# Optimization experiments

Measured on AMD Instinct MI355X. Metric: run time of the kernel, lower is better.

Reference implementation:

```python
import jax, jax.numpy as jnp
import numpy as np

B, T, U, D, H, V = 2, 512, 128, 512, 512, 1024

def setup_inputs() -> dict:
    key = jax.random.key(0)
    k1, k2, k3, k4 = jax.random.split(key, 4)
    pred_inp = jax.random.normal(k1, (B, U, D), dtype=jnp.float32)
    enc_inp = jax.random.normal(k2, (B, T, D), dtype=jnp.float32)
    W0 = jax.random.normal(k3, (D, H), dtype=jnp.float32) * (1.0 / np.sqrt(D))
    b0 = jnp.zeros((H,), dtype=jnp.float32)
    W1 = jax.random.normal(k4, (H, V), dtype=jnp.float32) * (1.0 / np.sqrt(H))
    b1 = jnp.zeros((V,), dtype=jnp.float32)
    return {"pred_inp": pred_inp, "enc_inp": enc_inp, "W0": W0, "b0": b0, "W1": W1, "b1": b1}

def reference(pred_inp, enc_inp, W0, b0, W1, b1):
    # broadcast-add: enc [B,T,1,D] + pred [B,1,U,D] -> [B,T,U,D]
    x = enc_inp[:, :, None, :] + pred_inp[:, None, :, :]
    # Dense(additional_size)
    h = jnp.einsum('btud,dh->btuh', x, W0) + b0
    # Dense(output_size)
    out = jnp.einsum('btuh,hv->btuv', h, W1) + b1
    return out
```

## Files before the change

### kernel.cpp

```cpp
#include <hip/hip_runtime.h>


typedef float vf4 __attribute__((ext_vector_type(4)));
typedef short bf16x8 __attribute__((ext_vector_type(8)));
typedef float f32x4 __attribute__((ext_vector_type(4)));
typedef unsigned short us4 __attribute__((ext_vector_type(4)));

#define PADK 40

__device__ __forceinline__ unsigned short f2bf(float f) {
    union { float f; unsigned u; } v; v.f = f;
    const unsigned r = v.u + 0x7FFFu + ((v.u >> 16) & 1u);
    return (unsigned short)(r >> 16);
}

template<bool A_BF16, bool C_BF16>
__global__ __launch_bounds__(256) void gemm_mfma(
    const void* __restrict__ Aptr, const float* __restrict__ A1,
    const float* __restrict__ Bmat,
    const float* __restrict__ biasv,
    void* __restrict__ Cptr, int N, int K)
{
    __shared__ unsigned short As[64 * PADK];
    __shared__ unsigned short Bst[64 * PADK];

    const int tid  = threadIdx.x;
    const int row0 = blockIdx.y * 64;
    const int col0 = blockIdx.x * 64;
    const int w    = tid >> 6;
    const int lane = tid & 63;
    const int l16  = lane & 15;
    const int kq   = lane >> 4;

    float4 ar[2]; bf16x8 ab; float4 br[2];

    auto loadA = [&](int kb) {
        if (A_BF16) {
            const unsigned short* A = (const unsigned short*)Aptr;
            const int r = tid >> 2, k8 = (tid & 3) << 3;
            ab = *reinterpret_cast<const bf16x8*>(A + (size_t)(row0 + r) * K + kb + k8);
        } else {
            #pragma unroll
            for (int i = 0; i < 2; ++i) {
                const int idx = tid + (i << 8);
                const int r = idx >> 3, k4 = (idx & 7) << 2;
                const float* Arow = (row0 < 1024)
                    ? (const float*)Aptr + (size_t)(row0 + r) * K
                    : A1 + (size_t)(row0 - 1024 + r) * K;
                ar[i] = *reinterpret_cast<const float4*>(Arow + kb + k4);
            }
        }
    };
    auto loadB = [&](int kb) {
        #pragma unroll
        for (int i = 0; i < 2; ++i) {
            const int idx = tid + (i << 8);
            const int kk = idx >> 4, n4 = (idx & 15) << 2;
            br[i] = *reinterpret_cast<const float4*>(Bmat + (size_t)(kb + kk) * N + col0 + n4);
        }
    };
    auto stage = [&]() {
        if (A_BF16) {
            const int r = tid >> 2, k8 = (tid & 3) << 3;
            *reinterpret_cast<bf16x8*>(&As[r * PADK + k8]) = ab;
        } else {
            #pragma unroll
            for (int i = 0; i < 2; ++i) {
                const int idx = tid + (i << 8);
                const int r = idx >> 3, k4 = (idx & 7) << 2;
                us4 p = { f2bf(ar[i].x), f2bf(ar[i].y), f2bf(ar[i].z), f2bf(ar[i].w) };
                *reinterpret_cast<us4*>(&As[r * PADK + k4]) = p;
            }
        }
        #pragma unroll
        for (int i = 0; i < 2; ++i) {
            const int idx = tid + (i << 8);
            const int kk = idx >> 4, n4 = (idx & 15) << 2;
            Bst[(n4 + 0) * PADK + kk] = f2bf(br[i].x);
            Bst[(n4 + 1) * PADK + kk] = f2bf(br[i].y);
            Bst[(n4 + 2) * PADK + kk] = f2bf(br[i].z);
            Bst[(n4 + 3) * PADK + kk] = f2bf(br[i].w);
        }
    };

    f32x4 acc[4] = {};
    const unsigned short* a_base = &As[(w * 16 + l16) * PADK + kq * 8];

    loadA(0); loadB(0);
    const int nkt = K >> 5;
    for (int kt = 0; kt < nkt; ++kt) {
        __syncthreads();
        stage();
        __syncthreads();
        if (kt + 1 < nkt) { loadA((kt + 1) << 5); loadB((kt + 1) << 5); }
        bf16x8 a = *reinterpret_cast<const bf16x8*>(a_base);
        #pragma unroll
        for (int nf = 0; nf < 4; ++nf) {
            bf16x8 b = *reinterpret_cast<const bf16x8*>(&Bst[(nf * 16 + l16) * PADK + kq * 8]);
            acc[nf] = __builtin_amdgcn_mfma_f32_16x16x32_bf16(a, b, acc[nf], 0, 0, 0);
        }
    }

    const int cr0 = row0 + w * 16 + kq * 4;
    const bool doBias = (row0 >= 1024);
    #pragma unroll
    for (int nf = 0; nf < 4; ++nf) {
        const int c = col0 + nf * 16 + l16;
        const float bv = doBias ? biasv[c] : 0.0f;
        #pragma unroll
        for (int r = 0; r < 4; ++r) {
            const float v = acc[nf][r] + bv;
            if (C_BF16) ((unsigned short*)Cptr)[(size_t)(cr0 + r) * N + c] = f2bf(v);
            else        ((float*)Cptr)[(size_t)(cr0 + r) * N + c] = v;
        }
    }
}

__global__ __launch_bounds__(256) void bcast_add(
    const vf4* __restrict__ Q, vf4* __restrict__ out)
{
    const int bid = blockIdx.x;
    const int bt = bid >> 1;
    const int uh = bid & 1;
    const int v4 = threadIdx.x;
    const int b = bt >> 9;

    const vf4 ye = Q[((size_t)bt << 8) + v4];
    const vf4* yp = Q + ((size_t)(1024 + b * 128 + uh * 64) << 8) + v4;
    vf4* o = out + (((size_t)bt * 128 + uh * 64) << 8) + v4;
    #pragma unroll 4
    for (int u = 0; u < 64; ++u) {
        __builtin_nontemporal_store(ye + yp[(size_t)u << 8], o + ((size_t)u << 8));
    }
}

extern "C" void kernel_launch(void* const* d_in, const int* in_sizes, int n_in,
                              void* d_out, int out_size, void* d_ws, size_t ws_size,
                              hipStream_t stream)
{
    const float* pred = (const float*)d_in[0];
    const float* enc  = (const float*)d_in[1];
    const float* W0   = (const float*)d_in[2];
    const float* b0   = (const float*)d_in[3];
    const float* W1   = (const float*)d_in[4];
    const float* b1   = (const float*)d_in[5];
    float* out = (float*)d_out;

    char* base = (char*)d_ws;
    unsigned short* P = (unsigned short*)base;
    float* Q = (float*)(base + (size_t)(1 << 21));

    gemm_mfma<false, true><<<dim3(8, 20), 256, 0, stream>>>(
        enc, pred, W0, b0, P, 512, 512);

    gemm_mfma<true, false><<<dim3(16, 20), 256, 0, stream>>>(
        P, nullptr, W1, b1, Q, 1024, 512);

    bcast_add<<<2048, 256, 0, stream>>>((const vf4*)Q, (vf4*)out);
}
```

Measured before the change: 129.6 us.

## Tile broadcast-add over 8 timesteps and 8 label rows per thread

Restructures the broadcast-add kernel so each block handles 8 encoder rows × 64 predictor rows × 32 vector columns. Each thread keeps 8 encoder and 8 predictor vectors in registers and produces 64 outputs. Before, every output needed a fresh predictor load; now each loaded vector is reused 8 times, cutting Q read traffic. The trade-off is more registers per thread and a different store pattern: contiguous runs per row drop from 4 KB to 512 B.

```diff
diff --git a/kernel.cpp b/kernel.cpp
--- a/kernel.cpp
+++ b/kernel.cpp
@@ -120,17 +120,31 @@
     const vf4* __restrict__ Q, vf4* __restrict__ out)
 {
     const int bid = blockIdx.x;
-    const int bt = bid >> 1;
-    const int uh = bid & 1;
-    const int v4 = threadIdx.x;
-    const int b = bt >> 9;
+    const int g   = bid >> 4;
+    const int uh  = (bid >> 3) & 1;
+    const int vt  = bid & 7;
+    const int bt0 = g << 3;
+    const int b   = bt0 >> 9;
+    const int u8  = threadIdx.x >> 5;
+    const int c4  = threadIdx.x & 31;
+    const int vcol = vt * 32 + c4;
 
-    const vf4 ye = Q[((size_t)bt << 8) + v4];
-    const vf4* yp = Q + ((size_t)(1024 + b * 128 + uh * 64) << 8) + v4;
-    vf4* o = out + (((size_t)bt * 128 + uh * 64) << 8) + v4;
-    #pragma unroll 4
-    for (int u = 0; u < 64; ++u) {
-        __builtin_nontemporal_store(ye + yp[(size_t)u << 8], o + ((size_t)u << 8));
+    vf4 ye[8], yp[8];
+    #pragma unroll
+    for (int i = 0; i < 8; ++i)
+        ye[i] = Q[(size_t)(bt0 + i) * 256 + vcol];
+    const int urow0 = 1024 + b * 128 + uh * 64 + u8 * 8;
+    #pragma unroll
+    for (int i = 0; i < 8; ++i)
+        yp[i] = Q[(size_t)(urow0 + i) * 256 + vcol];
+
+    #pragma unroll
+    for (int bt = 0; bt < 8; ++bt) {
+        vf4* o = out + ((size_t)(bt0 + bt) * 128 + uh * 64 + u8 * 8) * 256 + vcol;
+        #pragma unroll
+        for (int uu = 0; uu < 8; ++uu) {
+            __builtin_nontemporal_store(ye[bt] + yp[uu], o + (size_t)uu * 256);
+        }
     }
 }
 
```

Result: faster. 121.3 us (-6.4%).
